# Performance work log

Measured on AMD Instinct MI355X. Metric: run time of the kernel, lower is better.

## Reference

```python
import jax, jax.numpy as jnp
import numpy as np

N, E, D, R, L = 50000, 600000, 64, 65, 2


def setup_inputs() -> dict:
    key = jax.random.key(0)
    ks = jax.random.split(key, 10)
    x = jax.random.normal(ks[0], (N, D), dtype=jnp.float32)
    edge_index = jax.random.randint(ks[1], (2, E), 0, N, dtype=jnp.int64)
    edge_type = jax.random.randint(ks[2], (E,), 0, R, dtype=jnp.int64)
    s = 1.0 / np.sqrt(D)
    W = jax.random.normal(ks[3], (L, R, D, D), dtype=jnp.float32) * s
    root = jax.random.normal(ks[4], (L, D, D), dtype=jnp.float32) * s
    bias = jax.random.normal(ks[5], (L, D), dtype=jnp.float32) * 0.01
    res_W = jax.random.normal(ks[6], (L, D, D), dtype=jnp.float32) * s
    res_b = jax.random.normal(ks[7], (L, D), dtype=jnp.float32) * 0.01
    return {"x": x, "edge_index": edge_index, "edge_type": edge_type,
            "W": W, "root": root, "bias": bias, "res_W": res_W, "res_b": res_b}


def _rgcn_conv(x, src, dst, edge_type, W_r, W_root, b):
    # PyG RGCNConv (num_bases=None, aggr='mean'):
    #   out_i = x_i @ W_root + b + sum_r mean_{j in N_r(i)} (x_j @ W_r)
    # mean is linear, so aggregate raw features per (node, relation) first,
    # then apply the per-relation transform once per node.
    n, d = x.shape
    r = W_r.shape[0]
    seg = dst * r + edge_type                       # [E]
    msg = x[src]                                    # [E, D] gather
    agg = jax.ops.segment_sum(msg, seg, num_segments=n * r).reshape(n, r, d)
    cnt = jax.ops.segment_sum(jnp.ones((msg.shape[0],), x.dtype), seg,
                              num_segments=n * r).reshape(n, r, 1)
    mean = agg / jnp.maximum(cnt, 1.0)              # [N, R, D]
    out = jnp.einsum('nrd,rdk->nk', mean, W_r)
    return out + x @ W_root + b


def reference(x, edge_index, edge_type, W, root, bias, res_W, res_b):
    src, dst = edge_index[0], edge_index[1]
    h = x
    for l in range(W.shape[0]):
        conv = _rgcn_conv(h, src, dst, edge_type, W[l], root[l], bias[l])
        conv = jax.nn.relu(conv)
        # dropout: identity in eval mode
        res = jax.nn.relu(h @ res_W[l] + res_b[l])
        h = conv + res
    return h
```

## Files before the change

kernel.cpp:

```cpp
#include <hip/hip_runtime.h>


constexpr int NN  = 50000;
constexpr int EE  = 600000;
constexpr int DIM = 64;
constexpr int RR  = 65;
constexpr int CHUNK = 256;
constexpr int MAXCHUNKS = EE / CHUNK + RR + 8;
constexpr int SORT_BS = 2048;
constexpr int NSB = (EE + SORT_BS - 1) / SORT_BS;
constexpr int SCAN_BS = 1024;
constexpr int SCAN_NB = (NN + SCAN_BS - 1) / SCAN_BS;
constexpr int XNB = 64;

typedef __attribute__((ext_vector_type(8))) short short8v;
typedef __attribute__((ext_vector_type(4))) float floatx4;

__device__ inline unsigned short f2bf(float f) {
  unsigned int u = __float_as_uint(f);
  return (unsigned short)((u + 0x7fffu + ((u >> 16) & 1u)) >> 16);
}
__device__ inline float bf2f(unsigned short v) {
  return __uint_as_float(((unsigned int)v) << 16);
}


constexpr int ZN4 = NN * RR * 2 / 16;
constexpr int ZB  = (ZN4 + 255) / 256;
constexpr int CW4 = 2 * RR * DIM * DIM / 4;
constexpr int CB  = (CW4 + 255) / 256;
constexpr int HB  = (NN * DIM / 8 + 255) / 256;

__global__ __launch_bounds__(256) void setup_k(int4* __restrict__ zp,
                                               const float* __restrict__ W,
                                               unsigned short* __restrict__ WT,
                                               const float* __restrict__ x,
                                               unsigned short* __restrict__ hbf) {
  const int b = blockIdx.x;
  if (b < ZB) {
    const int i = b * 256 + threadIdx.x;
    if (i < ZN4) zp[i] = make_int4(0, 0, 0, 0);
  } else if (b < ZB + CB) {
    const int tid = (b - ZB) * 256 + threadIdx.x;
    if (tid >= CW4) return;
    const int base = tid * 4;
    const int mat = base >> 12, rem = base & 4095;
    const int k = rem >> 6, c0 = rem & 63;
    const float4 v = *reinterpret_cast<const float4*>(W + base);
    unsigned short* o = WT + (size_t)mat * 4096;
    o[(c0 + 0) * 64 + k] = f2bf(v.x);
    o[(c0 + 1) * 64 + k] = f2bf(v.y);
    o[(c0 + 2) * 64 + k] = f2bf(v.z);
    o[(c0 + 3) * 64 + k] = f2bf(v.w);
  } else {
    const int tid = (b - ZB - CB) * 256 + threadIdx.x;
    if (tid * 8 >= NN * DIM) return;
    const float4 v0 = reinterpret_cast<const float4*>(x)[tid * 2];
    const float4 v1 = reinterpret_cast<const float4*>(x)[tid * 2 + 1];
    ushort4 a, c;
    a.x = f2bf(v0.x); a.y = f2bf(v0.y); a.z = f2bf(v0.z); a.w = f2bf(v0.w);
    c.x = f2bf(v1.x); c.y = f2bf(v1.y); c.z = f2bf(v1.z); c.w = f2bf(v1.w);
    reinterpret_cast<ushort4*>(hbf)[tid * 2] = a;
    reinterpret_cast<ushort4*>(hbf)[tid * 2 + 1] = c;
  }
}

__global__ __launch_bounds__(512) void hist_k(const int* __restrict__ dst,
                                              const int* __restrict__ et,
                                              unsigned int* __restrict__ cnt32,
                                              int* __restrict__ bhist, int E) {
  __shared__ int lh[RR];
  if (threadIdx.x < RR) lh[threadIdx.x] = 0;
  __syncthreads();
  const int base = blockIdx.x * SORT_BS;
#pragma unroll
  for (int it = 0; it < SORT_BS / 512; ++it) {
    const int e = base + it * 512 + threadIdx.x;
    if (e < E) {
      const int d = dst[e], r = et[e];
      const int c = r * NN + d;
      atomicAdd(&cnt32[c >> 1], 1u << (16 * (c & 1)));
      atomicAdd(&lh[r], 1);
    }
  }
  __syncthreads();
  if (threadIdx.x < RR) bhist[blockIdx.x * RR + threadIdx.x] = lh[threadIdx.x];
}


__global__ __launch_bounds__(1024) void scanA_k(const unsigned short* __restrict__ c16,
                                                int* __restrict__ deg,
                                                int* __restrict__ bsum,
                                                const int* __restrict__ bhist,
                                                int* __restrict__ boffrel,
                                                int* __restrict__ total) {
  __shared__ int s[SCAN_BS];
  const int t = threadIdx.x;
  if (blockIdx.x < SCAN_NB) {
    const int idx = blockIdx.x * SCAN_BS + t;
    int d = 0;
    if (idx < NN) {
#pragma unroll 13
      for (int r = 0; r < RR; ++r) d += c16[r * NN + idx];
      deg[idx] = d;
    }
    s[t] = d;
    __syncthreads();
    for (int off = SCAN_BS / 2; off > 0; off >>= 1) {
      if (t < off) s[t] += s[t + off];
      __syncthreads();
    }
    if (t == 0) bsum[blockIdx.x] = s[0];
  } else {
    const int r = blockIdx.x - SCAN_NB;
    const int v = (t < NSB) ? bhist[t * RR + r] : 0;
    s[t] = v;
    __syncthreads();
    for (int off = 1; off < SCAN_BS; off <<= 1) {
      const int u = (t >= off) ? s[t - off] : 0;
      __syncthreads();
      s[t] += u;
      __syncthreads();
    }
    if (t < NSB) boffrel[t * RR + r] = s[t] - v;
    if (t == SCAN_BS - 1) total[r] = s[SCAN_BS - 1];
  }
}


__global__ __launch_bounds__(128) void scanB_k(int* __restrict__ bsum,
                                               const int* __restrict__ total,
                                               int* __restrict__ tptrg,
                                               int4* __restrict__ chunkArr,
                                               int* __restrict__ nchunks) {
  const int t = threadIdx.x;
  if (blockIdx.x == 0) {
    if (t < 64) {
      int v = (t < SCAN_NB) ? bsum[t] : 0;
      const int orig = v;
      for (int off = 1; off < 64; off <<= 1) {
        const int u = __shfl_up(v, off, 64);
        if (t >= off) v += u;
      }
      if (t < SCAN_NB) bsum[t] = v - orig;
    }
  } else {
    __shared__ int tptr[RR + 1], chbase[RR + 1];
    if (t == 0) {
      int run = 0, crun = 0;
      for (int r = 0; r < RR; ++r) {
        tptr[r] = run;    run  += total[r];
        chbase[r] = crun; crun += (total[r] + CHUNK - 1) / CHUNK;
      }
      tptr[RR] = run; chbase[RR] = crun;
      *nchunks = crun;
    }
    __syncthreads();
    if (t < RR) {
      tptrg[t] = tptr[t];
      const int tot = total[t];
      const int nc = (tot + CHUNK - 1) / CHUNK;
      for (int i = 0; i < nc; ++i) {
        const int beg = tptr[t] + i * CHUNK;
        chunkArr[chbase[t] + i] = make_int4(beg, min(beg + CHUNK, tptr[t] + tot), t, 0);
      }
    }
  }
}

__global__ __launch_bounds__(1024) void scan3_k(const int* __restrict__ deg,
                                                const int* __restrict__ bsum,
                                                int* __restrict__ rowptr,
                                                int* __restrict__ poscur) {
  __shared__ int s[SCAN_BS];
  const int t = threadIdx.x;
  const int idx = blockIdx.x * SCAN_BS + t;
  const int v = (idx < NN) ? deg[idx] : 0;
  s[t] = v;
  __syncthreads();
  for (int off = 1; off < SCAN_BS; off <<= 1) {
    const int u = (t >= off) ? s[t - off] : 0;
    __syncthreads();
    s[t] += u;
    __syncthreads();
  }
  const int excl = bsum[blockIdx.x] + s[t] - v;
  if (idx < NN) { rowptr[idx] = excl; poscur[idx] = excl; }
  if (idx == NN - 1) rowptr[NN] = EE;
}

__global__ __launch_bounds__(512) void scatter_k(const int* __restrict__ src,
                                                 const int* __restrict__ dst,
                                                 const int* __restrict__ et,
                                                 const unsigned short* __restrict__ c16,
                                                 const int* __restrict__ boffrel,
                                                 const int* __restrict__ tptrg,
                                                 int* __restrict__ poscur,
                                                 int* __restrict__ osrc,
                                                 int* __restrict__ opos,
                                                 float* __restrict__ oscale, int E) {
  __shared__ int cur[RR];
  if (threadIdx.x < RR)
    cur[threadIdx.x] = tptrg[threadIdx.x] + boffrel[blockIdx.x * RR + threadIdx.x];
  __syncthreads();
  const int base = blockIdx.x * SORT_BS;
#pragma unroll
  for (int it = 0; it < SORT_BS / 512; ++it) {
    const int e = base + it * 512 + threadIdx.x;
    if (e < E) {
      const int s = src[e], d = dst[e], r = et[e];
      const int q = atomicAdd(&cur[r], 1);
      const int p = atomicAdd(&poscur[d], 1);
      osrc[q] = s;
      opos[q] = p;
      oscale[q] = 1.0f / (float)c16[r * NN + d];
    }
  }
}


__global__ __launch_bounds__(256) void msgm_k(const unsigned short* __restrict__ hbf,
                                              const int* __restrict__ osrc,
                                              const int* __restrict__ opos,
                                              const float* __restrict__ oscale,
                                              const unsigned short* __restrict__ WT,
                                              const int4* __restrict__ chunkArr,
                                              const int* __restrict__ nchunks,
                                              unsigned short* __restrict__ m) {
  const int ci = blockIdx.x;
  if (ci >= *nchunks) return;
  const int4 c = chunkArr[ci];
  const int beg = c.x, end = c.y, rel = c.z;

  __shared__ unsigned short Wl[DIM][72];
  {
    const float4* s4 = reinterpret_cast<const float4*>(WT + (size_t)rel * 4096);
#pragma unroll
    for (int it = 0; it < 2; ++it) {
      const int seg = threadIdx.x + it * 256;
      const int row = seg >> 3, s8 = seg & 7;
      *reinterpret_cast<float4*>(&Wl[row][s8 * 8]) = s4[seg];
    }
  }
  __syncthreads();

  const int w  = threadIdx.x >> 6;
  const int l  = threadIdx.x & 63;
  const int lr = l & 15, lq = l >> 4;

  const int ebase = beg + w * 64;
  if (ebase >= end) return;

  short8v a[4][2];
#pragma unroll
  for (int ct = 0; ct < 4; ++ct)
#pragma unroll
    for (int kk = 0; kk < 2; ++kk)
      a[ct][kk] = *reinterpret_cast<const short8v*>(&Wl[ct * 16 + lr][kk * 32 + lq * 8]);

  short8v b[4][2];
  int eidx[4];
#pragma unroll
  for (int et = 0; et < 4; ++et) {
    eidx[et] = ebase + et * 16 + lr;
    const int e = min(eidx[et], end - 1);
    const int s = osrc[e];
    const unsigned short* hp = hbf + (size_t)s * DIM;
    b[et][0] = *reinterpret_cast<const short8v*>(hp + lq * 8);
    b[et][1] = *reinterpret_cast<const short8v*>(hp + 32 + lq * 8);
  }

  floatx4 acc[4][4];
#pragma unroll
  for (int ct = 0; ct < 4; ++ct)
#pragma unroll
    for (int et = 0; et < 4; ++et)
      acc[ct][et] = (floatx4){0.f, 0.f, 0.f, 0.f};

#pragma unroll
  for (int kk = 0; kk < 2; ++kk)
#pragma unroll
    for (int ct = 0; ct < 4; ++ct)
#pragma unroll
      for (int et = 0; et < 4; ++et)
        acc[ct][et] = __builtin_amdgcn_mfma_f32_16x16x32_bf16(a[ct][kk], b[et][kk],
                                                              acc[ct][et], 0, 0, 0);

#pragma unroll
  for (int et = 0; et < 4; ++et) {
    const int e = eidx[et];
    if (e < end) {
      const float sc = oscale[e];
      unsigned short* op = m + (size_t)opos[e] * DIM;
#pragma unroll
      for (int ct = 0; ct < 4; ++ct) {
        ushort4 o;
        o.x = f2bf(acc[ct][et][0] * sc);
        o.y = f2bf(acc[ct][et][1] * sc);
        o.z = f2bf(acc[ct][et][2] * sc);
        o.w = f2bf(acc[ct][et][3] * sc);
        *reinterpret_cast<ushort4*>(op + ct * 16 + lq * 4) = o;
      }
    }
  }
}

template<bool F32SRC>
__global__ __launch_bounds__(256) void xform_k(const void* __restrict__ hsrc,
                                               const float* __restrict__ root,
                                               const float* __restrict__ bias,
                                               const float* __restrict__ rw,
                                               const float* __restrict__ rb,
                                               unsigned short* __restrict__ rt16,
                                               unsigned short* __restrict__ rs16, int N) {
  __shared__ float Wl0[DIM * DIM];
  __shared__ float Wl1[DIM * DIM];
  __shared__ float xs[XNB][68];
#pragma unroll
  for (int i = 0; i < 4; ++i) {
    reinterpret_cast<float4*>(Wl0)[threadIdx.x + i * 256] =
        reinterpret_cast<const float4*>(root)[threadIdx.x + i * 256];
    reinterpret_cast<float4*>(Wl1)[threadIdx.x + i * 256] =
        reinterpret_cast<const float4*>(rw)[threadIdx.x + i * 256];
  }

  const int g = threadIdx.x >> 4, li = threadIdx.x & 15;
  const int base = blockIdx.x * XNB;
#pragma unroll
  for (int r = 0; r < 4; ++r) {
    const int n = base + g * 4 + r;
    float4 v = make_float4(0.f, 0.f, 0.f, 0.f);
    if (n < N) {
      if (F32SRC) {
        v = *reinterpret_cast<const float4*>((const float*)hsrc + (size_t)n * DIM + li * 4);
      } else {
        const ushort4 u = *reinterpret_cast<const ushort4*>(
            (const unsigned short*)hsrc + (size_t)n * DIM + li * 4);
        v = make_float4(bf2f(u.x), bf2f(u.y), bf2f(u.z), bf2f(u.w));
      }
    }
    *reinterpret_cast<float4*>(&xs[g * 4 + r][li * 4]) = v;
  }
  __syncthreads();

  float aR[4][4], aS[4][4];
#pragma unroll
  for (int r = 0; r < 4; ++r)
#pragma unroll
    for (int q = 0; q < 4; ++q) { aR[r][q] = 0.f; aS[r][q] = 0.f; }

#pragma unroll 4
  for (int k = 0; k < DIM; ++k) {
    const float4 wr = *reinterpret_cast<const float4*>(&Wl0[k * DIM + li * 4]);
    const float4 wv = *reinterpret_cast<const float4*>(&Wl1[k * DIM + li * 4]);
#pragma unroll
    for (int r = 0; r < 4; ++r) {
      const float xv = xs[g * 4 + r][k];
      aR[r][0] += xv * wr.x; aR[r][1] += xv * wr.y; aR[r][2] += xv * wr.z; aR[r][3] += xv * wr.w;
      aS[r][0] += xv * wv.x; aS[r][1] += xv * wv.y; aS[r][2] += xv * wv.z; aS[r][3] += xv * wv.w;
    }
  }

  const float4 bv = reinterpret_cast<const float4*>(bias)[li];
  const float4 cv = reinterpret_cast<const float4*>(rb)[li];
#pragma unroll
  for (int r = 0; r < 4; ++r) {
    const int n = base + g * 4 + r;
    if (n < N) {
      ushort4 t, s;
      t.x = f2bf(aR[r][0] + bv.x); t.y = f2bf(aR[r][1] + bv.y);
      t.z = f2bf(aR[r][2] + bv.z); t.w = f2bf(aR[r][3] + bv.w);
      s.x = f2bf(fmaxf(aS[r][0] + cv.x, 0.f)); s.y = f2bf(fmaxf(aS[r][1] + cv.y, 0.f));
      s.z = f2bf(fmaxf(aS[r][2] + cv.z, 0.f)); s.w = f2bf(fmaxf(aS[r][3] + cv.w, 0.f));
      *reinterpret_cast<ushort4*>(rt16 + (size_t)n * DIM + li * 4) = t;
      *reinterpret_cast<ushort4*>(rs16 + (size_t)n * DIM + li * 4) = s;
    }
  }
}

template<bool OUT_BF16>
__global__ __launch_bounds__(256) void gather2_k(const unsigned short* __restrict__ m,
                                                 const int* __restrict__ rowptr,
                                                 const unsigned short* __restrict__ rt16,
                                                 const unsigned short* __restrict__ rs16,
                                                 void* __restrict__ hout, int N) {
  const int g = threadIdx.x >> 4, li = threadIdx.x & 15;
  const int n = blockIdx.x * 16 + g;
  if (n >= N) return;

  float a0 = 0.f, a1 = 0.f, a2 = 0.f, a3 = 0.f;
  const int jb = rowptr[n], je = rowptr[n + 1];
  int j = jb;
  for (; j + 8 <= je; j += 8) {
    ushort4 v[8];
#pragma unroll
    for (int u = 0; u < 8; ++u)
      v[u] = *reinterpret_cast<const ushort4*>(m + (size_t)(j + u) * DIM + li * 4);
#pragma unroll
    for (int u = 0; u < 8; ++u) {
      a0 += bf2f(v[u].x); a1 += bf2f(v[u].y); a2 += bf2f(v[u].z); a3 += bf2f(v[u].w);
    }
  }
  for (; j + 4 <= je; j += 4) {
    ushort4 v[4];
#pragma unroll
    for (int u = 0; u < 4; ++u)
      v[u] = *reinterpret_cast<const ushort4*>(m + (size_t)(j + u) * DIM + li * 4);
#pragma unroll
    for (int u = 0; u < 4; ++u) {
      a0 += bf2f(v[u].x); a1 += bf2f(v[u].y); a2 += bf2f(v[u].z); a3 += bf2f(v[u].w);
    }
  }
  for (; j < je; ++j) {
    const ushort4 v = *reinterpret_cast<const ushort4*>(m + (size_t)j * DIM + li * 4);
    a0 += bf2f(v.x); a1 += bf2f(v.y); a2 += bf2f(v.z); a3 += bf2f(v.w);
  }

  const ushort4 tu = *reinterpret_cast<const ushort4*>(rt16 + (size_t)n * DIM + li * 4);
  const ushort4 su = *reinterpret_cast<const ushort4*>(rs16 + (size_t)n * DIM + li * 4);
  const float o0 = fmaxf(a0 + bf2f(tu.x), 0.f) + bf2f(su.x);
  const float o1 = fmaxf(a1 + bf2f(tu.y), 0.f) + bf2f(su.y);
  const float o2 = fmaxf(a2 + bf2f(tu.z), 0.f) + bf2f(su.z);
  const float o3 = fmaxf(a3 + bf2f(tu.w), 0.f) + bf2f(su.w);
  if (OUT_BF16) {
    ushort4 o;
    o.x = f2bf(o0); o.y = f2bf(o1); o.z = f2bf(o2); o.w = f2bf(o3);
    *reinterpret_cast<ushort4*>((unsigned short*)hout + (size_t)n * DIM + li * 4) = o;
  } else {
    *reinterpret_cast<float4*>((float*)hout + (size_t)n * DIM + li * 4) =
        make_float4(o0, o1, o2, o3);
  }
}


__global__ __launch_bounds__(256) void count_k(const int* __restrict__ dst,
                                               const int* __restrict__ et,
                                               int* __restrict__ cnt, int E) {
  int e = blockIdx.x * 256 + threadIdx.x;
  if (e < E) atomicAdd(&cnt[dst[e] * RR + et[e]], 1);
}

__global__ __launch_bounds__(256) void edge_k(const float* __restrict__ h,
                                              const int* __restrict__ src,
                                              const int* __restrict__ dst,
                                              const int* __restrict__ et,
                                              const float* __restrict__ W,
                                              const int* __restrict__ cnt,
                                              float* __restrict__ accum, int E) {
  __shared__ float xs[16][68];
  const int g = threadIdx.x >> 4, li = threadIdx.x & 15;
  const int e = blockIdx.x * 16 + g;
  if (e >= E) return;
  const int s = src[e], d = dst[e], t = et[e];
  *reinterpret_cast<float4*>(&xs[g][li * 4]) =
      *reinterpret_cast<const float4*>(h + (size_t)s * DIM + li * 4);
  const float* Wt = W + (size_t)t * (DIM * DIM) + li * 4;
  float a0 = 0.f, a1 = 0.f, a2 = 0.f, a3 = 0.f;
#pragma unroll 8
  for (int k = 0; k < DIM; ++k) {
    const float xd = xs[g][k];
    const float4 w = *reinterpret_cast<const float4*>(Wt + k * DIM);
    a0 += xd * w.x; a1 += xd * w.y; a2 += xd * w.z; a3 += xd * w.w;
  }
  const float sc = 1.0f / (float)cnt[d * RR + t];
  float* o = accum + (size_t)d * DIM + li * 4;
  unsafeAtomicAdd(o + 0, a0 * sc);
  unsafeAtomicAdd(o + 1, a1 * sc);
  unsafeAtomicAdd(o + 2, a2 * sc);
  unsafeAtomicAdd(o + 3, a3 * sc);
}

__global__ __launch_bounds__(256) void node_k(const float* __restrict__ h,
                                              const float* __restrict__ root,
                                              const float* __restrict__ bias,
                                              const float* __restrict__ rw,
                                              const float* __restrict__ rb,
                                              float* __restrict__ io, int N) {
  __shared__ float xs[16][68];
  const int g = threadIdx.x >> 4, li = threadIdx.x & 15;
  const int n = blockIdx.x * 16 + g;
  if (n >= N) return;
  *reinterpret_cast<float4*>(&xs[g][li * 4]) =
      *reinterpret_cast<const float4*>(h + (size_t)n * DIM + li * 4);
  float r0 = 0.f, r1 = 0.f, r2 = 0.f, r3 = 0.f;
  float s0 = 0.f, s1 = 0.f, s2 = 0.f, s3 = 0.f;
#pragma unroll 8
  for (int k = 0; k < DIM; ++k) {
    const float hd = xs[g][k];
    const float4 w = *reinterpret_cast<const float4*>(root + k * DIM + li * 4);
    const float4 v = *reinterpret_cast<const float4*>(rw + k * DIM + li * 4);
    r0 += hd * w.x; r1 += hd * w.y; r2 += hd * w.z; r3 += hd * w.w;
    s0 += hd * v.x; s1 += hd * v.y; s2 += hd * v.z; s3 += hd * v.w;
  }
  float* o = io + (size_t)n * DIM + li * 4;
  const float4 acc = *reinterpret_cast<const float4*>(o);
  const float4 b = *reinterpret_cast<const float4*>(bias + li * 4);
  const float4 c = *reinterpret_cast<const float4*>(rb + li * 4);
  float o0 = fmaxf(acc.x + r0 + b.x, 0.f) + fmaxf(s0 + c.x, 0.f);
  float o1 = fmaxf(acc.y + r1 + b.y, 0.f) + fmaxf(s1 + c.y, 0.f);
  float o2 = fmaxf(acc.z + r2 + b.z, 0.f) + fmaxf(s2 + c.z, 0.f);
  float o3 = fmaxf(acc.w + r3 + b.w, 0.f) + fmaxf(s3 + c.w, 0.f);
  *reinterpret_cast<float4*>(o) = make_float4(o0, o1, o2, o3);
}


extern "C" void kernel_launch(void* const* d_in, const int* in_sizes, int n_in,
                              void* d_out, int out_size, void* d_ws, size_t ws_size,
                              hipStream_t stream) {
  const float* x    = (const float*)d_in[0];
  const int*   ei   = (const int*)d_in[1];
  const int*   et   = (const int*)d_in[2];
  const float* W    = (const float*)d_in[3];
  const float* root = (const float*)d_in[4];
  const float* bias = (const float*)d_in[5];
  const float* resW = (const float*)d_in[6];
  const float* resb = (const float*)d_in[7];
  float* out = (float*)d_out;

  const int* src = ei;
  const int* dstp = ei + EE;

  char* ws = (char*)d_ws;
  size_t off = 0;
  auto take = [&](size_t bytes) -> void* {
    void* p = ws + off;
    off = (off + bytes + 255) & ~(size_t)255;
    return p;
  };
  unsigned short* m = (unsigned short*)take((size_t)EE * DIM * sizeof(unsigned short));
  int* deg       = (int*)take((size_t)NN * sizeof(int));
  int* rowptr    = (int*)take((size_t)(NN + 1) * sizeof(int));
  int* poscur    = (int*)take((size_t)NN * sizeof(int));
  int* bhist     = (int*)take((size_t)NSB * RR * sizeof(int));
  int* boffrel   = (int*)take((size_t)NSB * RR * sizeof(int));
  int* total     = (int*)take((size_t)RR * sizeof(int));
  int* tptrg     = (int*)take((size_t)RR * sizeof(int));
  int* bsum      = (int*)take((size_t)SCAN_NB * sizeof(int));
  int* osrc      = (int*)take((size_t)EE * sizeof(int));
  int* opos      = (int*)take((size_t)EE * sizeof(int));
  float* oscale  = (float*)take((size_t)EE * sizeof(float));
  int4* chunkArr = (int4*)take((size_t)MAXCHUNKS * sizeof(int4));
  int* nchunks   = (int*)take(256);
  unsigned short* rt16 = (unsigned short*)take((size_t)NN * DIM * sizeof(unsigned short));
  unsigned short* rs16 = (unsigned short*)take((size_t)NN * DIM * sizeof(unsigned short));
  unsigned short* hbf  = (unsigned short*)take((size_t)NN * DIM * sizeof(unsigned short));
  unsigned short* wbt  = (unsigned short*)take((size_t)2 * RR * DIM * DIM * sizeof(unsigned short));
  const size_t main_off = off;
  unsigned int* cnt32 = (unsigned int*)m;
  const unsigned short* c16 = (const unsigned short*)m;

  if (main_off <= ws_size) {
    setup_k<<<ZB + CB + HB, 256, 0, stream>>>((int4*)cnt32, W, wbt, x, hbf);
    hist_k<<<NSB, 512, 0, stream>>>(dstp, et, cnt32, bhist, EE);
    scanA_k<<<SCAN_NB + RR, 1024, 0, stream>>>(c16, deg, bsum, bhist, boffrel, total);
    scanB_k<<<2, 128, 0, stream>>>(bsum, total, tptrg, chunkArr, nchunks);
    scan3_k<<<SCAN_NB, 1024, 0, stream>>>(deg, bsum, rowptr, poscur);
    scatter_k<<<NSB, 512, 0, stream>>>(src, dstp, et, c16, boffrel, tptrg, poscur,
                                       osrc, opos, oscale, EE);

    const int XG = (NN + XNB - 1) / XNB;
    xform_k<true><<<XG, 256, 0, stream>>>(x, root, bias, resW, resb, rt16, rs16, NN);
    msgm_k<<<MAXCHUNKS, 256, 0, stream>>>(hbf, osrc, opos, oscale, wbt, chunkArr, nchunks, m);
    gather2_k<true><<<(NN + 15) / 16, 256, 0, stream>>>(m, rowptr, rt16, rs16, hbf, NN);
    xform_k<false><<<XG, 256, 0, stream>>>(hbf, root + DIM * DIM, bias + DIM,
                                           resW + DIM * DIM, resb + DIM, rt16, rs16, NN);
    msgm_k<<<MAXCHUNKS, 256, 0, stream>>>(hbf, osrc, opos, oscale,
                                          wbt + (size_t)RR * DIM * DIM, chunkArr, nchunks, m);
    gather2_k<false><<<(NN + 15) / 16, 256, 0, stream>>>(m, rowptr, rt16, rs16, out, NN);
  } else {
    int* fcnt = (int*)ws;
    float* fh1 = (float*)(ws + (size_t)NN * RR * sizeof(int));
    hipMemsetAsync(fcnt, 0, (size_t)NN * RR * sizeof(int), stream);
    hipMemsetAsync(fh1, 0, (size_t)NN * DIM * sizeof(float), stream);
    hipMemsetAsync(out, 0, (size_t)NN * DIM * sizeof(float), stream);
    count_k<<<(EE + 255) / 256, 256, 0, stream>>>(dstp, et, fcnt, EE);
    edge_k<<<(EE + 15) / 16, 256, 0, stream>>>(x, src, dstp, et, W, fcnt, fh1, EE);
    node_k<<<(NN + 15) / 16, 256, 0, stream>>>(x, root, bias, resW, resb, fh1, NN);
    edge_k<<<(EE + 15) / 16, 256, 0, stream>>>(fh1, src, dstp, et,
                                               W + (size_t)RR * DIM * DIM, fcnt, out, EE);
    node_k<<<(NN + 15) / 16, 256, 0, stream>>>(fh1, root + DIM * DIM, bias + DIM,
                                               resW + DIM * DIM, resb + DIM, out, NN);
  }
}
```

Measured before the change: 230.2 us.

## Replace dense per-(node,relation) count table with per-node degree and local scale

Drops the dense N×R 16-bit count table, so its zeroing, the hist atomics into it, and the 65-way column reduction in scanA go away. Only a per-node degree is now accumulated. A new scale_k kernel computes each edge's 1/count by scanning its destination's CSR row quadratically over the relation ids that scatter now writes. The scale is applied in the gather kernels rather than in msgm, which adds an extra per-edge float read there. This assumes degrees stay small, which holds for the random graph with about 12 edges per node.

```diff
diff --git a/kernel.cpp b/kernel.cpp
--- a/kernel.cpp
+++ b/kernel.cpp
@@ -25,7 +25,7 @@
 }
 
 
-constexpr int ZN4 = NN * RR * 2 / 16;
+constexpr int ZN4 = (NN + 3) / 4;
 constexpr int ZB  = (ZN4 + 255) / 256;
 constexpr int CW4 = 2 * RR * DIM * DIM / 4;
 constexpr int CB  = (CW4 + 255) / 256;
@@ -67,7 +67,7 @@
 
 __global__ __launch_bounds__(512) void hist_k(const int* __restrict__ dst,
                                               const int* __restrict__ et,
-                                              unsigned int* __restrict__ cnt32,
+                                              int* __restrict__ deg,
                                               int* __restrict__ bhist, int E) {
   __shared__ int lh[RR];
   if (threadIdx.x < RR) lh[threadIdx.x] = 0;
@@ -77,10 +77,8 @@
   for (int it = 0; it < SORT_BS / 512; ++it) {
     const int e = base + it * 512 + threadIdx.x;
     if (e < E) {
-      const int d = dst[e], r = et[e];
-      const int c = r * NN + d;
-      atomicAdd(&cnt32[c >> 1], 1u << (16 * (c & 1)));
-      atomicAdd(&lh[r], 1);
+      atomicAdd(&deg[dst[e]], 1);
+      atomicAdd(&lh[et[e]], 1);
     }
   }
   __syncthreads();
@@ -88,8 +86,7 @@
 }
 
 
-__global__ __launch_bounds__(1024) void scanA_k(const unsigned short* __restrict__ c16,
-                                                int* __restrict__ deg,
+__global__ __launch_bounds__(1024) void scanA_k(const int* __restrict__ deg,
                                                 int* __restrict__ bsum,
                                                 const int* __restrict__ bhist,
                                                 int* __restrict__ boffrel,
@@ -98,13 +95,7 @@
   const int t = threadIdx.x;
   if (blockIdx.x < SCAN_NB) {
     const int idx = blockIdx.x * SCAN_BS + t;
-    int d = 0;
-    if (idx < NN) {
-#pragma unroll 13
-      for (int r = 0; r < RR; ++r) d += c16[r * NN + idx];
-      deg[idx] = d;
-    }
-    s[t] = d;
+    s[t] = (idx < NN) ? deg[idx] : 0;
     __syncthreads();
     for (int off = SCAN_BS / 2; off > 0; off >>= 1) {
       if (t < off) s[t] += s[t + off];
@@ -192,13 +183,12 @@
 __global__ __launch_bounds__(512) void scatter_k(const int* __restrict__ src,
                                                  const int* __restrict__ dst,
                                                  const int* __restrict__ et,
-                                                 const unsigned short* __restrict__ c16,
                                                  const int* __restrict__ boffrel,
                                                  const int* __restrict__ tptrg,
                                                  int* __restrict__ poscur,
                                                  int* __restrict__ osrc,
                                                  int* __restrict__ opos,
-                                                 float* __restrict__ oscale, int E) {
+                                                 int* __restrict__ orel, int E) {
   __shared__ int cur[RR];
   if (threadIdx.x < RR)
     cur[threadIdx.x] = tptrg[threadIdx.x] + boffrel[blockIdx.x * RR + threadIdx.x];
@@ -213,8 +203,22 @@
       const int p = atomicAdd(&poscur[d], 1);
       osrc[q] = s;
       opos[q] = p;
-      oscale[q] = 1.0f / (float)c16[r * NN + d];
-    }
+      orel[p] = r;
+    }
+  }
+}
+
+__global__ __launch_bounds__(256) void scale_k(const int* __restrict__ rowptr,
+                                               const int* __restrict__ orel,
+                                               float* __restrict__ sc, int N) {
+  const int n = blockIdx.x * 256 + threadIdx.x;
+  if (n >= N) return;
+  const int jb = rowptr[n], je = rowptr[n + 1];
+  for (int j1 = jb; j1 < je; ++j1) {
+    const int r1 = orel[j1];
+    int c = 0;
+    for (int j2 = jb; j2 < je; ++j2) c += (orel[j2] == r1) ? 1 : 0;
+    sc[j1] = 1.0f / (float)c;
   }
 }
 
@@ -222,7 +226,6 @@
 __global__ __launch_bounds__(256) void msgm_k(const unsigned short* __restrict__ hbf,
                                               const int* __restrict__ osrc,
                                               const int* __restrict__ opos,
-                                              const float* __restrict__ oscale,
                                               const unsigned short* __restrict__ WT,
                                               const int4* __restrict__ chunkArr,
                                               const int* __restrict__ nchunks,
@@ -290,15 +293,14 @@
   for (int et = 0; et < 4; ++et) {
     const int e = eidx[et];
     if (e < end) {
-      const float sc = oscale[e];
       unsigned short* op = m + (size_t)opos[e] * DIM;
 #pragma unroll
       for (int ct = 0; ct < 4; ++ct) {
         ushort4 o;
-        o.x = f2bf(acc[ct][et][0] * sc);
-        o.y = f2bf(acc[ct][et][1] * sc);
-        o.z = f2bf(acc[ct][et][2] * sc);
-        o.w = f2bf(acc[ct][et][3] * sc);
+        o.x = f2bf(acc[ct][et][0]);
+        o.y = f2bf(acc[ct][et][1]);
+        o.z = f2bf(acc[ct][et][2]);
+        o.w = f2bf(acc[ct][et][3]);
         *reinterpret_cast<ushort4*>(op + ct * 16 + lq * 4) = o;
       }
     }
@@ -379,7 +381,8 @@
 }
 
 template<bool OUT_BF16>
-__global__ __launch_bounds__(256) void gather2_k(const unsigned short* __restrict__ m,
+__global__ __launch_bounds__(256) void gather3_k(const unsigned short* __restrict__ m,
+                                                 const float* __restrict__ sc,
                                                  const int* __restrict__ rowptr,
                                                  const unsigned short* __restrict__ rt16,
                                                  const unsigned short* __restrict__ rs16,
@@ -393,27 +396,36 @@
   int j = jb;
   for (; j + 8 <= je; j += 8) {
     ushort4 v[8];
-#pragma unroll
-    for (int u = 0; u < 8; ++u)
+    float cc[8];
+#pragma unroll
+    for (int u = 0; u < 8; ++u) {
       v[u] = *reinterpret_cast<const ushort4*>(m + (size_t)(j + u) * DIM + li * 4);
+      cc[u] = sc[j + u];
+    }
 #pragma unroll
     for (int u = 0; u < 8; ++u) {
-      a0 += bf2f(v[u].x); a1 += bf2f(v[u].y); a2 += bf2f(v[u].z); a3 += bf2f(v[u].w);
+      a0 += cc[u] * bf2f(v[u].x); a1 += cc[u] * bf2f(v[u].y);
+      a2 += cc[u] * bf2f(v[u].z); a3 += cc[u] * bf2f(v[u].w);
     }
   }
   for (; j + 4 <= je; j += 4) {
     ushort4 v[4];
-#pragma unroll
-    for (int u = 0; u < 4; ++u)
+    float cc[4];
+#pragma unroll
+    for (int u = 0; u < 4; ++u) {
       v[u] = *reinterpret_cast<const ushort4*>(m + (size_t)(j + u) * DIM + li * 4);
+      cc[u] = sc[j + u];
+    }
 #pragma unroll
     for (int u = 0; u < 4; ++u) {
-      a0 += bf2f(v[u].x); a1 += bf2f(v[u].y); a2 += bf2f(v[u].z); a3 += bf2f(v[u].w);
+      a0 += cc[u] * bf2f(v[u].x); a1 += cc[u] * bf2f(v[u].y);
+      a2 += cc[u] * bf2f(v[u].z); a3 += cc[u] * bf2f(v[u].w);
     }
   }
   for (; j < je; ++j) {
+    const float cc = sc[j];
     const ushort4 v = *reinterpret_cast<const ushort4*>(m + (size_t)j * DIM + li * 4);
-    a0 += bf2f(v.x); a1 += bf2f(v.y); a2 += bf2f(v.z); a3 += bf2f(v.w);
+    a0 += cc * bf2f(v.x); a1 += cc * bf2f(v.y); a2 += cc * bf2f(v.z); a3 += cc * bf2f(v.w);
   }
 
   const ushort4 tu = *reinterpret_cast<const ushort4*>(rt16 + (size_t)n * DIM + li * 4);
@@ -528,7 +540,7 @@
     return p;
   };
   unsigned short* m = (unsigned short*)take((size_t)EE * DIM * sizeof(unsigned short));
-  int* deg       = (int*)take((size_t)NN * sizeof(int));
+  int* deg       = (int*)take((size_t)((NN + 3) & ~3) * sizeof(int));
   int* rowptr    = (int*)take((size_t)(NN + 1) * sizeof(int));
   int* poscur    = (int*)take((size_t)NN * sizeof(int));
   int* bhist     = (int*)take((size_t)NSB * RR * sizeof(int));
@@ -538,7 +550,8 @@
   int* bsum      = (int*)take((size_t)SCAN_NB * sizeof(int));
   int* osrc      = (int*)take((size_t)EE * sizeof(int));
   int* opos      = (int*)take((size_t)EE * sizeof(int));
-  float* oscale  = (float*)take((size_t)EE * sizeof(float));
+  int* orel      = (int*)take((size_t)EE * sizeof(int));
+  float* sc      = (float*)take((size_t)EE * sizeof(float));
   int4* chunkArr = (int4*)take((size_t)MAXCHUNKS * sizeof(int4));
   int* nchunks   = (int*)take(256);
   unsigned short* rt16 = (unsigned short*)take((size_t)NN * DIM * sizeof(unsigned short));
@@ -546,27 +559,26 @@
   unsigned short* hbf  = (unsigned short*)take((size_t)NN * DIM * sizeof(unsigned short));
   unsigned short* wbt  = (unsigned short*)take((size_t)2 * RR * DIM * DIM * sizeof(unsigned short));
   const size_t main_off = off;
-  unsigned int* cnt32 = (unsigned int*)m;
-  const unsigned short* c16 = (const unsigned short*)m;
 
   if (main_off <= ws_size) {
-    setup_k<<<ZB + CB + HB, 256, 0, stream>>>((int4*)cnt32, W, wbt, x, hbf);
-    hist_k<<<NSB, 512, 0, stream>>>(dstp, et, cnt32, bhist, EE);
-    scanA_k<<<SCAN_NB + RR, 1024, 0, stream>>>(c16, deg, bsum, bhist, boffrel, total);
+    setup_k<<<ZB + CB + HB, 256, 0, stream>>>((int4*)deg, W, wbt, x, hbf);
+    hist_k<<<NSB, 512, 0, stream>>>(dstp, et, deg, bhist, EE);
+    scanA_k<<<SCAN_NB + RR, 1024, 0, stream>>>(deg, bsum, bhist, boffrel, total);
     scanB_k<<<2, 128, 0, stream>>>(bsum, total, tptrg, chunkArr, nchunks);
     scan3_k<<<SCAN_NB, 1024, 0, stream>>>(deg, bsum, rowptr, poscur);
-    scatter_k<<<NSB, 512, 0, stream>>>(src, dstp, et, c16, boffrel, tptrg, poscur,
-                                       osrc, opos, oscale, EE);
+    scatter_k<<<NSB, 512, 0, stream>>>(src, dstp, et, boffrel, tptrg, poscur,
+                                       osrc, opos, orel, EE);
+    scale_k<<<(NN + 255) / 256, 256, 0, stream>>>(rowptr, orel, sc, NN);
 
     const int XG = (NN + XNB - 1) / XNB;
     xform_k<true><<<XG, 256, 0, stream>>>(x, root, bias, resW, resb, rt16, rs16, NN);
-    msgm_k<<<MAXCHUNKS, 256, 0, stream>>>(hbf, osrc, opos, oscale, wbt, chunkArr, nchunks, m);
-    gather2_k<true><<<(NN + 15) / 16, 256, 0, stream>>>(m, rowptr, rt16, rs16, hbf, NN);
+    msgm_k<<<MAXCHUNKS, 256, 0, stream>>>(hbf, osrc, opos, wbt, chunkArr, nchunks, m);
+    gather3_k<true><<<(NN + 15) / 16, 256, 0, stream>>>(m, sc, rowptr, rt16, rs16, hbf, NN);
     xform_k<false><<<XG, 256, 0, stream>>>(hbf, root + DIM * DIM, bias + DIM,
                                            resW + DIM * DIM, resb + DIM, rt16, rs16, NN);
-    msgm_k<<<MAXCHUNKS, 256, 0, stream>>>(hbf, osrc, opos, oscale,
+    msgm_k<<<MAXCHUNKS, 256, 0, stream>>>(hbf, osrc, opos,
                                           wbt + (size_t)RR * DIM * DIM, chunkArr, nchunks, m);
-    gather2_k<false><<<(NN + 15) / 16, 256, 0, stream>>>(m, rowptr, rt16, rs16, out, NN);
+    gather3_k<false><<<(NN + 15) / 16, 256, 0, stream>>>(m, sc, rowptr, rt16, rs16, out, NN);
   } else {
     int* fcnt = (int*)ws;
     float* fh1 = (float*)(ws + (size_t)NN * RR * sizeof(int));
```

Result: slower. 282.1 us (+22.6%).
